# Performance work log

Measured on AMD Instinct MI355X. Metric: run time of the kernel, lower is better.

Reference implementation:

```python
import jax, jax.numpy as jnp
import numpy as np

DIM = 2048
HEADS = 16
HEAD_DIM = 128
B = 2
T = 2048


def _rope_as_in_source(x):
    # x: (b, h, t, d). FAITHFUL to the source bug: RotaryEmbedding uses
    # x.shape[1] (the HEADS axis, since it is called after transpose) as the
    # 'sequence' index, so rotation angle depends on head index and is
    # broadcast over the true sequence axis.
    n = x.shape[1]  # == heads
    d = x.shape[-1]
    inv_freq = 1.0 / (10000.0 ** (jnp.arange(0, d, 2, dtype=jnp.float32) / d))
    freqs = jnp.arange(n, dtype=jnp.float32)[:, None] * inv_freq[None, :]  # (h, d/2)
    cos = jnp.cos(freqs)[None, :, None, :]  # (1, h, 1, d/2)
    sin = jnp.sin(freqs)[None, :, None, :]
    x1 = x[..., 0::2]
    x2 = x[..., 1::2]
    out = jnp.stack([x1 * cos - x2 * sin, x1 * sin + x2 * cos], axis=-1)
    return out.reshape(x.shape)


def setup_inputs() -> dict:
    key = jax.random.key(0)
    ks = jax.random.split(key, 9)
    s_in = 1.0 / np.sqrt(DIM)
    hd = HEADS * HEAD_DIM
    s_o = 1.0 / np.sqrt(hd)
    return {
        "x": jax.random.normal(ks[0], (B, T, DIM), dtype=jnp.float32),
        "Wq": jax.random.normal(ks[1], (DIM, hd), dtype=jnp.float32) * s_in,
        "bq": jnp.zeros((hd,), dtype=jnp.float32),
        "Wk": jax.random.normal(ks[2], (DIM, hd), dtype=jnp.float32) * s_in,
        "bk": jnp.zeros((hd,), dtype=jnp.float32),
        "Wv": jax.random.normal(ks[3], (DIM, hd), dtype=jnp.float32) * s_in,
        "bv": jnp.zeros((hd,), dtype=jnp.float32),
        "Wo": jax.random.normal(ks[4], (hd, DIM), dtype=jnp.float32) * s_o,
        "bo": jnp.zeros((DIM,), dtype=jnp.float32),
    }


def reference(x, Wq, bq, Wk, bk, Wv, bv, Wo, bo):
    b, t, c = x.shape
    q = (x @ Wq + bq).reshape(b, t, HEADS, HEAD_DIM).transpose(0, 2, 1, 3)
    k = (x @ Wk + bk).reshape(b, t, HEADS, HEAD_DIM).transpose(0, 2, 1, 3)
    v = (x @ Wv + bv).reshape(b, t, HEADS, HEAD_DIM).transpose(0, 2, 1, 3)
    q = _rope_as_in_source(q)
    k = _rope_as_in_source(k)
    scale = 1.0 / np.sqrt(HEAD_DIM)
    scores = jnp.einsum("bhqd,bhkd->bhqk", q, k) * scale  # (b,h,t,t)
    attn = jax.nn.softmax(scores, axis=-1)
    out = jnp.einsum("bhqk,bhkd->bhqd", attn, v)  # (b,h,t,d)
    out = out.transpose(0, 2, 1, 3).reshape(b, t, HEADS * HEAD_DIM)
    return out @ Wo + bo
```

## Files before the change

### kernel.cpp

```cpp
#include <hip/hip_runtime.h>

typedef unsigned short ushort_t;
typedef unsigned int uint_t;
typedef __attribute__((ext_vector_type(8))) short short8;
typedef __attribute__((ext_vector_type(4))) float f32x4;
typedef __attribute__((ext_vector_type(4))) unsigned short ushort4_t;
typedef __attribute__((ext_vector_type(4))) unsigned int uint4_t;

__device__ inline float b2f(ushort_t u) {
    unsigned int x = ((unsigned int)u) << 16;
    return __builtin_bit_cast(float, x);
}
__device__ inline ushort_t f2b(float f) {
    unsigned int x = __builtin_bit_cast(unsigned int, f);
    x += 0x7fffu + ((x >> 16) & 1u);
    return (ushort_t)(x >> 16);
}
__device__ inline uint_t cvt_pk_bf16(float lo, float hi) {
    uint_t r;
    asm("v_cvt_pk_bf16_f32 %0, %1, %2" : "=v"(r) : "v"(lo), "v"(hi));
    return r;
}

__device__ inline void gload16(const void* g, void* l) {
    __builtin_amdgcn_global_load_lds(
        (const __attribute__((address_space(1))) void*)g,
        (__attribute__((address_space(3))) void*)l, 16, 0, 0);
}

__global__ __launch_bounds__(256)
void cast_bf16(const float* __restrict__ src, ushort_t* __restrict__ dst) {
    size_t i = ((size_t)blockIdx.x * 256 + threadIdx.x) * 8;
    f32x4 a = *reinterpret_cast<const f32x4*>(src + i);
    f32x4 b = *reinterpret_cast<const f32x4*>(src + i + 4);
    short8 v;
#pragma unroll
    for (int j = 0; j < 4; ++j) { v[j] = (short)f2b(a[j]); v[4 + j] = (short)f2b(b[j]); }
    *reinterpret_cast<short8*>(dst + i) = v;
}

__global__ __launch_bounds__(64)
void transp4(const float* __restrict__ s0, const float* __restrict__ s1,
             const float* __restrict__ s2, const float* __restrict__ s3,
             ushort_t* __restrict__ d0, ushort_t* __restrict__ d1,
             ushort_t* __restrict__ d2, ushort_t* __restrict__ d3) {
    const int z = blockIdx.z;
    const float* src = (z == 0) ? s0 : (z == 1) ? s1 : (z == 2) ? s2 : s3;
    ushort_t* dst = (z == 0) ? d0 : (z == 1) ? d1 : (z == 2) ? d2 : d3;
    const int R = 2048, C = 2048;
    int r0 = blockIdx.x * 64 + ((threadIdx.x >> 3) << 3);
    int c0 = blockIdx.y * 64 + ((threadIdx.x & 7) << 3);
    ushort_t v[8][8];
#pragma unroll
    for (int i = 0; i < 8; ++i) {
        const float* p = src + (size_t)(r0 + i) * C + c0;
        f32x4 a = *reinterpret_cast<const f32x4*>(p);
        f32x4 b = *reinterpret_cast<const f32x4*>(p + 4);
#pragma unroll
        for (int j = 0; j < 4; ++j) { v[i][j] = f2b(a[j]); v[i][4 + j] = f2b(b[j]); }
    }
#pragma unroll
    for (int c = 0; c < 8; ++c) {
        short8 w;
#pragma unroll
        for (int i = 0; i < 8; ++i) w[i] = (short)v[i][c];
        *reinterpret_cast<short8*>(dst + (size_t)(c0 + c) * R + r0) = w;
    }
}

__global__ __launch_bounds__(64)
void transp_v(const ushort_t* __restrict__ src, ushort_t* __restrict__ dst, int R, int C) {
    src += (size_t)blockIdx.z * R * C;
    dst += (size_t)blockIdx.z * R * C;
    int r0 = blockIdx.x * 64 + ((threadIdx.x >> 3) << 3);
    int c0 = blockIdx.y * 64 + ((threadIdx.x & 7) << 3);
    ushort_t v[8][8];
#pragma unroll
    for (int i = 0; i < 8; ++i) {
        short8 a = *reinterpret_cast<const short8*>(src + (size_t)(r0 + i) * C + c0);
#pragma unroll
        for (int j = 0; j < 8; ++j) v[i][j] = (ushort_t)a[j];
    }
#pragma unroll
    for (int c = 0; c < 8; ++c) {
        short8 w;
#pragma unroll
        for (int i = 0; i < 8; ++i) w[i] = (short)v[i][c];
        *reinterpret_cast<short8*>(dst + (size_t)(c0 + c) * R + r0) = w;
    }
}

template <bool BHTD, bool ROPE>
__global__ __launch_bounds__(256)
void gemm_bt(const ushort_t* __restrict__ A, const ushort_t* __restrict__ Bt,
             const float* __restrict__ bias, void* __restrict__ Cv,
             int M, int N, int K, float oscale) {
    __shared__ __align__(16) ushort_t As[128 * 64];
    __shared__ __align__(16) ushort_t Bs[128 * 64];
    const int tid = threadIdx.x, lane = tid & 63, wid = tid >> 6;
    const int l15 = lane & 15, g = lane >> 4;
    const int wr = wid >> 1, wc = wid & 1;
    const int m0 = blockIdx.y * 128, n0 = blockIdx.x * 128;
    f32x4 acc[4][4] = {};
    for (int k0 = 0; k0 < K; k0 += 64) {
#pragma unroll
        for (int is = 0; is < 4; ++is) {
            int c = is * 256 + tid;
            int row = c >> 3, sub = c & 7;
            int ks = (sub ^ (row & 7)) << 3;
            char* ldst = (char*)As + (size_t)(is * 256 + wid * 64) * 16;
            gload16(A + (size_t)(m0 + row) * K + k0 + ks, ldst);
            char* ldstB = (char*)Bs + (size_t)(is * 256 + wid * 64) * 16;
            gload16(Bt + (size_t)(n0 + row) * K + k0 + ks, ldstB);
        }
        __syncthreads();
#pragma unroll
        for (int kk = 0; kk < 2; ++kk) {
            short8 af[4], bf[4];
#pragma unroll
            for (int i = 0; i < 4; ++i) {
                int ra = wr * 64 + i * 16 + l15;
                af[i] = *reinterpret_cast<const short8*>(
                    (const char*)As + ra * 128 + (((4 * kk + g) ^ (ra & 7)) << 4));
                int rb = wc * 64 + i * 16 + l15;
                bf[i] = *reinterpret_cast<const short8*>(
                    (const char*)Bs + rb * 128 + (((4 * kk + g) ^ (rb & 7)) << 4));
            }
#pragma unroll
            for (int i = 0; i < 4; ++i)
#pragma unroll
                for (int j = 0; j < 4; ++j)
                    acc[i][j] = __builtin_amdgcn_mfma_f32_16x16x32_bf16(af[i], bf[j], acc[i][j], 0, 0, 0);
        }
        __syncthreads();
    }
#pragma unroll
    for (int j = 0; j < 4; ++j) {
        int n = n0 + wc * 64 + j * 16 + l15;
        float bj = bias[n];
        float sn = 0.f, cs = 1.f, sgn = 0.f;
        if (ROPE) {
            int d = n & 127, h = (n >> 7) & 15;
            float inv = expf(-(float)(d >> 1) * (9.210340371976184f / 64.0f));
            sincosf((float)h * inv, &sn, &cs);
            sgn = (d & 1) ? sn : -sn;
        }
#pragma unroll
        for (int i = 0; i < 4; ++i) {
            int mbase = m0 + wr * 64 + i * 16 + g * 4;
#pragma unroll
            for (int r = 0; r < 4; ++r) {
                int m = mbase + r;
                float v = acc[i][j][r] + bj;
                if (ROPE) {
                    float p = __shfl_xor(v, 1, 64);
                    v = fmaf(p, sgn, v * cs);
                    v *= oscale;
                }
                if (BHTD) {
                    size_t addr = ((size_t)((m >> 11) * 16 + (n >> 7)) * 2048 + (m & 2047)) * 128 + (n & 127);
                    ((ushort_t*)Cv)[addr] = f2b(v);
                } else {
                    ((float*)Cv)[(size_t)m * N + n] = v;
                }
            }
        }
    }
}

__global__ __launch_bounds__(512)
void fattn(const ushort_t* __restrict__ Q, const ushort_t* __restrict__ K,
           const ushort_t* __restrict__ Vt, ushort_t* __restrict__ O) {
    __shared__ __align__(16) ushort_t Ks[2][64 * 128];
    __shared__ __align__(16) ushort_t Vs[2][128 * 64];
    const int tid = threadIdx.x, lane = tid & 63, wid = tid >> 6;
    const int l15 = lane & 15, g = lane >> 4;
    const int h = blockIdx.y, b = blockIdx.z;
    const size_t base = ((size_t)b * 16 + h) * (2048 * 128);
    const int q0 = blockIdx.x * 128 + wid * 16;
    short8 qf[4];
#pragma unroll
    for (int c = 0; c < 4; ++c)
        qf[c] = *reinterpret_cast<const short8*>(Q + base + (size_t)(q0 + l15) * 128 + c * 32 + g * 8);
    f32x4 oacc[8] = {};
    f32x4 oaccL = {};
    float m_r = -__builtin_inff();
    short8 ones;
#pragma unroll
    for (int j = 0; j < 8; ++j) ones[j] = (short)0x3F80;
    const int addrA = ((32 * (g & 1)) + l15) << 2;
    const int addrB = addrA + 64;
    const bool hi = (lane & 32) != 0;

    auto stage = [&](int kv0, int bsel) {
#pragma unroll
        for (int is = 0; is < 2; ++is) {
            {
                int c = is * 512 + tid;
                int row = c >> 4, sub = c & 15;
                int dsrc = (sub ^ (row & 7)) << 3;
                gload16(K + base + (size_t)(kv0 + row) * 128 + dsrc,
                        (char*)Ks[bsel] + (size_t)c * 16);
            }
            {
                int c = is * 512 + tid;
                int row = c >> 3, sub = c & 7;
                int tsrc = (sub ^ (row & 7)) << 3;
                gload16(Vt + base + (size_t)row * 2048 + kv0 + tsrc,
                        (char*)Vs[bsel] + (size_t)c * 16);
            }
        }
    };

    stage(0, 0);
    asm volatile("s_waitcnt vmcnt(0)" ::: "memory");
    __builtin_amdgcn_s_barrier();

    for (int it = 0; it < 32; ++it) {
        const int cur = it & 1;
        if (it < 31) stage((it + 1) << 6, cur ^ 1);
        f32x4 s[4] = {};
        __builtin_amdgcn_s_setprio(1);
#pragma unroll
        for (int nt = 0; nt < 4; ++nt) {
            int kvr = nt * 16 + l15;
#pragma unroll
            for (int c = 0; c < 4; ++c) {
                short8 kf = *reinterpret_cast<const short8*>(
                    (const char*)Ks[cur] + kvr * 256 + (((4 * c + g) ^ (kvr & 7)) << 4));
                s[nt] = __builtin_amdgcn_mfma_f32_16x16x32_bf16(kf, qf[c], s[nt], 0, 0, 0);
            }
        }
        __builtin_amdgcn_s_setprio(0);
        float pm = fmaxf(fmaxf(fmaxf(s[0][0], s[0][1]), fmaxf(s[0][2], s[0][3])),
                         fmaxf(fmaxf(s[1][0], s[1][1]), fmaxf(s[1][2], s[1][3])));
        pm = fmaxf(pm, fmaxf(fmaxf(fmaxf(s[2][0], s[2][1]), fmaxf(s[2][2], s[2][3])),
                             fmaxf(fmaxf(s[3][0], s[3][1]), fmaxf(s[3][2], s[3][3]))));
        pm = fmaxf(pm, __shfl_xor(pm, 16, 64));
        pm = fmaxf(pm, __shfl_xor(pm, 32, 64));
        if (!__all(pm <= m_r + 5.0f)) {
            float mn = fmaxf(m_r, pm);
            float fac = exp2f(m_r - mn);
            m_r = mn;
#pragma unroll
            for (int r = 0; r < 4; ++r) oaccL[r] *= fac;
#pragma unroll
            for (int nt2 = 0; nt2 < 8; ++nt2)
#pragma unroll
                for (int r = 0; r < 4; ++r) oacc[nt2][r] *= fac;
        }
        uint_t W[4][2];
#pragma unroll
        for (int nt = 0; nt < 4; ++nt) {
            float p0 = exp2f(s[nt][0] - m_r);
            float p1 = exp2f(s[nt][1] - m_r);
            float p2 = exp2f(s[nt][2] - m_r);
            float p3 = exp2f(s[nt][3] - m_r);
            W[nt][0] = cvt_pk_bf16(p0, p1);
            W[nt][1] = cvt_pk_bf16(p2, p3);
        }
        __builtin_amdgcn_s_setprio(1);
#pragma unroll
        for (int ks = 0; ks < 2; ++ks) {
            uint_t xa, xb, w0, w1, w2, w3;
            xa = (uint_t)__builtin_amdgcn_ds_bpermute(addrA, (int)W[2 * ks][0]);
            xb = (uint_t)__builtin_amdgcn_ds_bpermute(addrA, (int)W[2 * ks + 1][0]);
            w0 = hi ? xb : xa;
            xa = (uint_t)__builtin_amdgcn_ds_bpermute(addrA, (int)W[2 * ks][1]);
            xb = (uint_t)__builtin_amdgcn_ds_bpermute(addrA, (int)W[2 * ks + 1][1]);
            w1 = hi ? xb : xa;
            xa = (uint_t)__builtin_amdgcn_ds_bpermute(addrB, (int)W[2 * ks][0]);
            xb = (uint_t)__builtin_amdgcn_ds_bpermute(addrB, (int)W[2 * ks + 1][0]);
            w2 = hi ? xb : xa;
            xa = (uint_t)__builtin_amdgcn_ds_bpermute(addrB, (int)W[2 * ks][1]);
            xb = (uint_t)__builtin_amdgcn_ds_bpermute(addrB, (int)W[2 * ks + 1][1]);
            w3 = hi ? xb : xa;
            uint4_t wv; wv[0] = w0; wv[1] = w1; wv[2] = w2; wv[3] = w3;
            short8 pb = __builtin_bit_cast(short8, wv);
            oaccL = __builtin_amdgcn_mfma_f32_16x16x32_bf16(ones, pb, oaccL, 0, 0, 0);
#pragma unroll
            for (int nt2 = 0; nt2 < 8; ++nt2) {
                int dr = nt2 * 16 + l15;
                short8 vb = *reinterpret_cast<const short8*>(
                    (const char*)Vs[cur] + dr * 128 + (((ks * 4 + g) ^ (dr & 7)) << 4));
                oacc[nt2] = __builtin_amdgcn_mfma_f32_16x16x32_bf16(vb, pb, oacc[nt2], 0, 0, 0);
            }
        }
        __builtin_amdgcn_s_setprio(0);
        asm volatile("s_waitcnt vmcnt(0)" ::: "memory");
        __builtin_amdgcn_s_barrier();
    }
    float lall = __shfl(oaccL[0], l15, 64);
    float inv = 1.f / lall;
    const size_t orow = ((size_t)b * 2048 + q0 + l15) * 2048 + (size_t)h * 128;
#pragma unroll
    for (int nt2 = 0; nt2 < 8; ++nt2) {
        ushort4_t w;
#pragma unroll
        for (int r = 0; r < 4; ++r) w[r] = f2b(oacc[nt2][r] * inv);
        *reinterpret_cast<ushort4_t*>(O + orow + nt2 * 16 + g * 4) = w;
    }
}

extern "C" void kernel_launch(void* const* d_in, const int* in_sizes, int n_in,
                              void* d_out, int out_size, void* d_ws, size_t ws_size,
                              hipStream_t stream) {
    const float* x  = (const float*)d_in[0];
    const float* Wq = (const float*)d_in[1];
    const float* bq = (const float*)d_in[2];
    const float* Wk = (const float*)d_in[3];
    const float* bk = (const float*)d_in[4];
    const float* Wv = (const float*)d_in[5];
    const float* bv = (const float*)d_in[6];
    const float* Wo = (const float*)d_in[7];
    const float* bo = (const float*)d_in[8];
    float* out = (float*)d_out;
    ushort_t* ws  = (ushort_t*)d_ws;

    const size_t WSZ = 2048ull * 2048;
    const size_t TSZ = 2ull * 16 * 2048 * 128;
    ushort_t* xb  = ws;
    ushort_t* Wtq = xb + TSZ;
    ushort_t* Wtk = Wtq + WSZ;
    ushort_t* Wtv = Wtk + WSZ;
    ushort_t* Wto = Wtv + WSZ;
    ushort_t* Qb  = Wto + WSZ;
    ushort_t* Kb  = Qb + TSZ;
    ushort_t* Vtb = Kb + TSZ;
    ushort_t* Sb  = Vtb + TSZ;

    const float QSC = 0.08838834764831845f * 1.4426950408889634f;

    cast_bf16<<<dim3(4096), 256, 0, stream>>>(x, xb);
    transp4<<<dim3(32, 32, 4), 64, 0, stream>>>(Wq, Wk, Wv, Wo, Wtq, Wtk, Wtv, Wto);

    gemm_bt<true, true ><<<dim3(16, 32), 256, 0, stream>>>(xb, Wtq, bq, Qb, 4096, 2048, 2048, QSC);
    gemm_bt<true, true ><<<dim3(16, 32), 256, 0, stream>>>(xb, Wtk, bk, Kb, 4096, 2048, 2048, 1.0f);
    gemm_bt<true, false><<<dim3(16, 32), 256, 0, stream>>>(xb, Wtv, bv, Sb, 4096, 2048, 2048, 1.0f);

    transp_v<<<dim3(32, 2, 32), 64, 0, stream>>>(Sb, Vtb, 2048, 128);

    fattn<<<dim3(16, 16, 2), 512, 0, stream>>>(Qb, Kb, Vtb, Sb);

    gemm_bt<false, false><<<dim3(16, 32), 256, 0, stream>>>(Sb, Wto, bo, out, 4096, 2048, 2048, 1.0f);
}
```

Baseline: 320.2 us.

## Fuse Q/K/V projections into one launch and write V transposed directly

Merges the three projection GEMMs into a single grid with blockIdx.z selecting Q, K or V, which gives more concurrent blocks and removes two launches. The V epilogue now writes the transposed (b,h,d,t) layout with vector stores, so the separate transp_v kernel and its round trip through memory are gone. The output GEMM becomes a specialised kernel, and the attention epilogue drops a shuffle by reading the row sum directly from the lane's accumulator. The risks are divergence from runtime z checks in the epilogue and the correctness of skipping the shuffle.

```diff
diff --git a/kernel.cpp b/kernel.cpp
--- a/kernel.cpp
+++ b/kernel.cpp
@@ -7,10 +7,6 @@
 typedef __attribute__((ext_vector_type(4))) unsigned short ushort4_t;
 typedef __attribute__((ext_vector_type(4))) unsigned int uint4_t;
 
-__device__ inline float b2f(ushort_t u) {
-    unsigned int x = ((unsigned int)u) << 16;
-    return __builtin_bit_cast(float, x);
-}
 __device__ inline ushort_t f2b(float f) {
     unsigned int x = __builtin_bit_cast(unsigned int, f);
     x += 0x7fffu + ((x >> 16) & 1u);
@@ -68,33 +64,20 @@
     }
 }
 
-__global__ __launch_bounds__(64)
-void transp_v(const ushort_t* __restrict__ src, ushort_t* __restrict__ dst, int R, int C) {
-    src += (size_t)blockIdx.z * R * C;
-    dst += (size_t)blockIdx.z * R * C;
-    int r0 = blockIdx.x * 64 + ((threadIdx.x >> 3) << 3);
-    int c0 = blockIdx.y * 64 + ((threadIdx.x & 7) << 3);
-    ushort_t v[8][8];
-#pragma unroll
-    for (int i = 0; i < 8; ++i) {
-        short8 a = *reinterpret_cast<const short8*>(src + (size_t)(r0 + i) * C + c0);
-#pragma unroll
-        for (int j = 0; j < 8; ++j) v[i][j] = (ushort_t)a[j];
-    }
-#pragma unroll
-    for (int c = 0; c < 8; ++c) {
-        short8 w;
-#pragma unroll
-        for (int i = 0; i < 8; ++i) w[i] = (short)v[i][c];
-        *reinterpret_cast<short8*>(dst + (size_t)(c0 + c) * R + r0) = w;
-    }
-}
-
-template <bool BHTD, bool ROPE>
 __global__ __launch_bounds__(256)
-void gemm_bt(const ushort_t* __restrict__ A, const ushort_t* __restrict__ Bt,
-             const float* __restrict__ bias, void* __restrict__ Cv,
-             int M, int N, int K, float oscale) {
+void gemm_qkv(const ushort_t* __restrict__ A,
+              const ushort_t* __restrict__ Btq, const ushort_t* __restrict__ Btk,
+              const ushort_t* __restrict__ Btv,
+              const float* __restrict__ bqp, const float* __restrict__ bkp,
+              const float* __restrict__ bvp,
+              ushort_t* __restrict__ Qb, ushort_t* __restrict__ Kb,
+              ushort_t* __restrict__ Vtb, float qsc) {
+    const int z = blockIdx.z;
+    const ushort_t* Bt = (z == 0) ? Btq : (z == 1) ? Btk : Btv;
+    const float* bias = (z == 0) ? bqp : (z == 1) ? bkp : bvp;
+    ushort_t* C = (z == 0) ? Qb : (z == 1) ? Kb : Vtb;
+    const float oscale = (z == 0) ? qsc : 1.0f;
+    const int K = 2048;
     __shared__ __align__(16) ushort_t As[128 * 64];
     __shared__ __align__(16) ushort_t Bs[128 * 64];
     const int tid = threadIdx.x, lane = tid & 63, wid = tid >> 6;
@@ -139,7 +122,7 @@
         int n = n0 + wc * 64 + j * 16 + l15;
         float bj = bias[n];
         float sn = 0.f, cs = 1.f, sgn = 0.f;
-        if (ROPE) {
+        if (z < 2) {
             int d = n & 127, h = (n >> 7) & 15;
             float inv = expf(-(float)(d >> 1) * (9.210340371976184f / 64.0f));
             sincosf((float)h * inv, &sn, &cs);
@@ -148,22 +131,83 @@
 #pragma unroll
         for (int i = 0; i < 4; ++i) {
             int mbase = m0 + wr * 64 + i * 16 + g * 4;
-#pragma unroll
-            for (int r = 0; r < 4; ++r) {
-                int m = mbase + r;
-                float v = acc[i][j][r] + bj;
-                if (ROPE) {
+            if (z == 2) {
+                int d = n & 127, hh = n >> 7;
+                int b_ = mbase >> 11, t0 = mbase & 2047;
+                ushort4_t w;
+#pragma unroll
+                for (int r = 0; r < 4; ++r) w[r] = f2b(acc[i][j][r] + bj);
+                *reinterpret_cast<ushort4_t*>(
+                    C + (((size_t)(b_ * 16 + hh) * 128 + d) * 2048 + t0)) = w;
+            } else {
+#pragma unroll
+                for (int r = 0; r < 4; ++r) {
+                    int m = mbase + r;
+                    float v = acc[i][j][r] + bj;
                     float p = __shfl_xor(v, 1, 64);
                     v = fmaf(p, sgn, v * cs);
                     v *= oscale;
+                    size_t addr = ((size_t)((m >> 11) * 16 + (n >> 7)) * 2048 + (m & 2047)) * 128 + (n & 127);
+                    C[addr] = f2b(v);
                 }
-                if (BHTD) {
-                    size_t addr = ((size_t)((m >> 11) * 16 + (n >> 7)) * 2048 + (m & 2047)) * 128 + (n & 127);
-                    ((ushort_t*)Cv)[addr] = f2b(v);
-                } else {
-                    ((float*)Cv)[(size_t)m * N + n] = v;
-                }
-            }
+            }
+        }
+    }
+}
+
+__global__ __launch_bounds__(256)
+void gemm_out(const ushort_t* __restrict__ A, const ushort_t* __restrict__ Bt,
+              const float* __restrict__ bias, float* __restrict__ C,
+              int M, int N, int K) {
+    __shared__ __align__(16) ushort_t As[128 * 64];
+    __shared__ __align__(16) ushort_t Bs[128 * 64];
+    const int tid = threadIdx.x, lane = tid & 63, wid = tid >> 6;
+    const int l15 = lane & 15, g = lane >> 4;
+    const int wr = wid >> 1, wc = wid & 1;
+    const int m0 = blockIdx.y * 128, n0 = blockIdx.x * 128;
+    f32x4 acc[4][4] = {};
+    for (int k0 = 0; k0 < K; k0 += 64) {
+#pragma unroll
+        for (int is = 0; is < 4; ++is) {
+            int c = is * 256 + tid;
+            int row = c >> 3, sub = c & 7;
+            int ks = (sub ^ (row & 7)) << 3;
+            char* ldst = (char*)As + (size_t)(is * 256 + wid * 64) * 16;
+            gload16(A + (size_t)(m0 + row) * K + k0 + ks, ldst);
+            char* ldstB = (char*)Bs + (size_t)(is * 256 + wid * 64) * 16;
+            gload16(Bt + (size_t)(n0 + row) * K + k0 + ks, ldstB);
+        }
+        __syncthreads();
+#pragma unroll
+        for (int kk = 0; kk < 2; ++kk) {
+            short8 af[4], bf[4];
+#pragma unroll
+            for (int i = 0; i < 4; ++i) {
+                int ra = wr * 64 + i * 16 + l15;
+                af[i] = *reinterpret_cast<const short8*>(
+                    (const char*)As + ra * 128 + (((4 * kk + g) ^ (ra & 7)) << 4));
+                int rb = wc * 64 + i * 16 + l15;
+                bf[i] = *reinterpret_cast<const short8*>(
+                    (const char*)Bs + rb * 128 + (((4 * kk + g) ^ (rb & 7)) << 4));
+            }
+#pragma unroll
+            for (int i = 0; i < 4; ++i)
+#pragma unroll
+                for (int j = 0; j < 4; ++j)
+                    acc[i][j] = __builtin_amdgcn_mfma_f32_16x16x32_bf16(af[i], bf[j], acc[i][j], 0, 0, 0);
+        }
+        __syncthreads();
+    }
+#pragma unroll
+    for (int j = 0; j < 4; ++j) {
+        int n = n0 + wc * 64 + j * 16 + l15;
+        float bj = bias[n];
+#pragma unroll
+        for (int i = 0; i < 4; ++i) {
+            int mbase = m0 + wr * 64 + i * 16 + g * 4;
+#pragma unroll
+            for (int r = 0; r < 4; ++r)
+                C[(size_t)(mbase + r) * N + n] = acc[i][j][r] + bj;
         }
     }
 }
@@ -290,8 +334,7 @@
         asm volatile("s_waitcnt vmcnt(0)" ::: "memory");
         __builtin_amdgcn_s_barrier();
     }
-    float lall = __shfl(oaccL[0], l15, 64);
-    float inv = 1.f / lall;
+    float inv = 1.f / oaccL[0];
     const size_t orow = ((size_t)b * 2048 + q0 + l15) * 2048 + (size_t)h * 128;
 #pragma unroll
     for (int nt2 = 0; nt2 < 8; ++nt2) {
@@ -334,13 +377,10 @@
     cast_bf16<<<dim3(4096), 256, 0, stream>>>(x, xb);
     transp4<<<dim3(32, 32, 4), 64, 0, stream>>>(Wq, Wk, Wv, Wo, Wtq, Wtk, Wtv, Wto);
 
-    gemm_bt<true, true ><<<dim3(16, 32), 256, 0, stream>>>(xb, Wtq, bq, Qb, 4096, 2048, 2048, QSC);
-    gemm_bt<true, true ><<<dim3(16, 32), 256, 0, stream>>>(xb, Wtk, bk, Kb, 4096, 2048, 2048, 1.0f);
-    gemm_bt<true, false><<<dim3(16, 32), 256, 0, stream>>>(xb, Wtv, bv, Sb, 4096, 2048, 2048, 1.0f);
-
-    transp_v<<<dim3(32, 2, 32), 64, 0, stream>>>(Sb, Vtb, 2048, 128);
+    gemm_qkv<<<dim3(16, 32, 3), 256, 0, stream>>>(xb, Wtq, Wtk, Wtv, bq, bk, bv,
+                                                  Qb, Kb, Vtb, QSC);
 
     fattn<<<dim3(16, 16, 2), 512, 0, stream>>>(Qb, Kb, Vtb, Sb);
 
-    gemm_bt<false, false><<<dim3(16, 32), 256, 0, stream>>>(Sb, Wto, bo, out, 4096, 2048, 2048, 1.0f);
-}
+    gemm_out<<<dim3(16, 32), 256, 0, stream>>>(Sb, Wto, bo, out, 4096, 2048, 2048);
+}
```

Result: no change. 315.0 us (-1.6%).
